# Kernel optimization log

Hardware: AMD Instinct MI355X
Metric: run time of the kernel (lower is better)

Reference implementation:

```python
import jax, jax.numpy as jnp
import numpy as np

N_NODES = 100000
N_EDGES = 1600000
D = 128
D_FF = 2 * D
BN_EPS = 1e-5


def setup_inputs() -> dict:
    key = jax.random.key(0)
    ks = jax.random.split(key, 16)
    s = lambda k, shp, fan: jax.random.normal(k, shp, jnp.float32) / np.float32(np.sqrt(fan))
    return {
        "x": jax.random.normal(ks[0], (N_NODES, D), jnp.float32),
        "edge_attr": jax.random.normal(ks[1], (N_EDGES, D), jnp.float32),
        "w1g": s(ks[2], (D, D), D),
        "b1g": jnp.zeros((D,), jnp.float32),
        "w2g": s(ks[3], (D, D), D),
        "b2g": jnp.zeros((D,), jnp.float32),
        "bn1_g": jax.random.uniform(ks[4], (D,), jnp.float32, 0.5, 1.5),
        "bn1_b": 0.1 * jax.random.normal(ks[5], (D,), jnp.float32),
        "ff_w1": s(ks[6], (D, D_FF), D),
        "ff_b1": jnp.zeros((D_FF,), jnp.float32),
        "ff_w2": s(ks[7], (D_FF, D), D_FF),
        "ff_b2": jnp.zeros((D,), jnp.float32),
        "bn2_g": jax.random.uniform(ks[8], (D,), jnp.float32, 0.5, 1.5),
        "bn2_b": 0.1 * jax.random.normal(ks[9], (D,), jnp.float32),
        "edge_index": jax.random.randint(ks[10], (2, N_EDGES), 0, N_NODES, jnp.int64 if jax.config.jax_enable_x64 else jnp.int32),
    }


def _batchnorm(h, gamma, beta):
    # training-mode BatchNorm1d: per-batch (node-axis) stats, biased variance
    mean = h.mean(axis=0)
    var = ((h - mean) ** 2).mean(axis=0)
    return gamma * (h - mean) * jax.lax.rsqrt(var + BN_EPS) + beta


def reference(x, edge_attr, w1g, b1g, w2g, b2g, bn1_g, bn1_b,
              ff_w1, ff_b1, ff_w2, ff_b2, bn2_g, bn2_b, edge_index):
    src, dst = edge_index[0], edge_index[1]
    # GINEConv message: relu(x_j + e_ij), scatter-sum into target nodes
    msg = jax.nn.relu(x[src] + edge_attr)                      # [E, D]
    agg = jax.ops.segment_sum(msg, dst, num_segments=N_NODES)  # [N, D]
    h = x + agg                                                # (1+eps)*x with eps=0
    # gin_nn: Linear -> ReLU -> Linear
    h = jax.nn.relu(h @ w1g + b1g) @ w2g + b2g
    h = jax.nn.relu(h)                                         # post-conv relu; dropout=identity (eval)
    h = x + h                                                  # residual
    h = _batchnorm(h, bn1_g, bn1_b)                            # norm1_local
    ff = jax.nn.relu(h @ ff_w1 + ff_b1) @ ff_w2 + ff_b2        # FFN block (dropouts identity)
    h = h + ff
    h = _batchnorm(h, bn2_g, bn2_b)                            # norm2
    return h
```

## Files before the change

kernel.cpp:

```cpp
#include <hip/hip_runtime.h>
#include <hip/hip_bf16.h>

#define NN 100000
#define NE 1600000
#define DD 128
#define DFF 256
#define BN_EPS 1e-5f
#define NND ((size_t)NN * DD)
#define NB_SCAN 391
#define NTILE 6250

typedef __attribute__((ext_vector_type(8))) short short8;
typedef __attribute__((ext_vector_type(4))) float f32x4;
typedef __attribute__((ext_vector_type(4))) unsigned short us4;

static __device__ __forceinline__ unsigned short f2bf(float f) {
  union { float f; unsigned u; } v; v.f = f;
  unsigned r = v.u + 0x7fffu + ((v.u >> 16) & 1u);
  return (unsigned short)(r >> 16);
}
static __device__ __forceinline__ float bf2f(unsigned short h) {
  union { unsigned u; float f; } v; v.u = ((unsigned)h) << 16;
  return v.f;
}

__global__ __launch_bounds__(256) void k_prep_misc(const float* __restrict__ x,
    unsigned short* __restrict__ xbf,
    const float* __restrict__ w1g, const float* __restrict__ w2g,
    const float* __restrict__ ffw1, const float* __restrict__ ffw2,
    unsigned short* __restrict__ w1t, unsigned short* __restrict__ w2t,
    unsigned short* __restrict__ fw1t, unsigned short* __restrict__ fw2t) {
  int b = blockIdx.x;
  if (b < 6250) {
    size_t base = ((size_t)b * 256u + threadIdx.x) * 8;
    const f32x4* xp = reinterpret_cast<const f32x4*>(x + base);
    f32x4 a0 = xp[0], a1 = xp[1];
    short8 o;
#pragma unroll
    for (int j = 0; j < 4; ++j) o[j] = (short)f2bf(a0[j]);
#pragma unroll
    for (int j = 0; j < 4; ++j) o[4 + j] = (short)f2bf(a1[j]);
    *reinterpret_cast<short8*>(xbf + base) = o;
  } else {
    int i = (b - 6250) * 256 + threadIdx.x;
    if (i < 16384) { int c = i & 127, k = i >> 7; w1t[c * 128 + k] = f2bf(w1g[k * 128 + c]); }
    else if (i < 32768) { i -= 16384; int c = i & 127, k = i >> 7; w2t[c * 128 + k] = f2bf(w2g[k * 128 + c]); }
    else if (i < 65536) { i -= 32768; int c = i & 255, k = i >> 8; fw1t[c * 128 + k] = f2bf(ffw1[k * 256 + c]); }
    else if (i < 98304) { i -= 65536; int c = i & 127, k = i >> 7; fw2t[c * 256 + k] = f2bf(ffw2[k * 128 + c]); }
  }
}

__global__ __launch_bounds__(256) void k_hist(const int* __restrict__ ei,
                                              int* __restrict__ cnt) {
  int e = blockIdx.x * 256 + threadIdx.x;
  if (e >= NE) return;
  atomicAdd(&cnt[ei[NE + e]], 1);
}

__global__ __launch_bounds__(256) void k_scan1(const int* __restrict__ cnt,
                                               int* __restrict__ bsum) {
  __shared__ int sh[256];
  int n = blockIdx.x * 256 + threadIdx.x;
  sh[threadIdx.x] = (n < NN) ? cnt[n] : 0;
  __syncthreads();
  for (int off = 128; off > 0; off >>= 1) {
    if (threadIdx.x < off) sh[threadIdx.x] += sh[threadIdx.x + off];
    __syncthreads();
  }
  if (threadIdx.x == 0) bsum[blockIdx.x] = sh[0];
}

__global__ __launch_bounds__(512) void k_scan2(const int* __restrict__ bsum,
                                               int* __restrict__ bpre,
                                               int* __restrict__ rs) {
  __shared__ int sh[512];
  int t = threadIdx.x;
  int v = (t < NB_SCAN) ? bsum[t] : 0;
  sh[t] = v;
  __syncthreads();
  for (int off = 1; off < 512; off <<= 1) {
    int u = (t >= off) ? sh[t - off] : 0;
    __syncthreads();
    sh[t] += u;
    __syncthreads();
  }
  if (t < NB_SCAN) bpre[t] = sh[t] - v;
  if (t == NB_SCAN - 1) rs[NN] = sh[t];
}

__global__ __launch_bounds__(256) void k_scan3(int* __restrict__ rs,
                                               const int* __restrict__ bpre,
                                               int* __restrict__ cursor) {
  __shared__ int sh[256];
  int n = blockIdx.x * 256 + threadIdx.x;
  int t = threadIdx.x;
  int v = (n < NN) ? rs[n] : 0;
  sh[t] = v;
  __syncthreads();
  for (int off = 1; off < 256; off <<= 1) {
    int u = (t >= off) ? sh[t - off] : 0;
    __syncthreads();
    sh[t] += u;
    __syncthreads();
  }
  if (n < NN) {
    int ex = bpre[blockIdx.x] + sh[t] - v;
    rs[n] = ex;
    cursor[n] = ex;
  }
}

__global__ __launch_bounds__(256) void k_scatter(const int* __restrict__ ei,
                                                 int* __restrict__ cursor,
                                                 int2* __restrict__ el2) {
  int e = blockIdx.x * 256 + threadIdx.x;
  if (e >= NE) return;
  int s = ei[e], d = ei[NE + e];
  int p = atomicAdd(&cursor[d], 1);
  el2[p] = make_int2(e, s);
}

__global__ __launch_bounds__(256) void k_gather(const float* __restrict__ x,
    const unsigned short* __restrict__ xbf, const float* __restrict__ ea,
    const int* __restrict__ rs, const int2* __restrict__ el2,
    unsigned short* __restrict__ h0) {
  int n = blockIdx.x * 8 + (threadIdx.x >> 5);
  int q = threadIdx.x & 31;
  int beg = rs[n], end = rs[n + 1];
  f32x4 acc = (f32x4){0.f, 0.f, 0.f, 0.f};
  int2 A = make_int2(0, 0), B = A;
  if (beg < end) A = el2[beg];
  if (beg + 1 < end) B = el2[beg + 1];
  int i = beg;
  for (; i + 2 <= end; i += 2) {
    f32x4 evA = *(reinterpret_cast<const f32x4*>(ea + (size_t)A.x * DD) + q);
    us4  xvA = *reinterpret_cast<const us4*>(xbf + (size_t)A.y * DD + q * 4);
    f32x4 evB = *(reinterpret_cast<const f32x4*>(ea + (size_t)B.x * DD) + q);
    us4  xvB = *reinterpret_cast<const us4*>(xbf + (size_t)B.y * DD + q * 4);
    int2 C = A, Dn = B;
    if (i + 2 < end) C = el2[i + 2];
    if (i + 3 < end) Dn = el2[i + 3];
#pragma unroll
    for (int c = 0; c < 4; ++c) {
      float mA = bf2f((unsigned short)xvA[c]) + evA[c];
      acc[c] += (mA > 0.f) ? mA : 0.f;
      float mB = bf2f((unsigned short)xvB[c]) + evB[c];
      acc[c] += (mB > 0.f) ? mB : 0.f;
    }
    A = C; B = Dn;
  }
  if (i < end) {
    f32x4 evA = *(reinterpret_cast<const f32x4*>(ea + (size_t)A.x * DD) + q);
    us4  xvA = *reinterpret_cast<const us4*>(xbf + (size_t)A.y * DD + q * 4);
#pragma unroll
    for (int c = 0; c < 4; ++c) {
      float mA = bf2f((unsigned short)xvA[c]) + evA[c];
      acc[c] += (mA > 0.f) ? mA : 0.f;
    }
  }
  f32x4 xn = *(reinterpret_cast<const f32x4*>(x + (size_t)n * DD) + q);
  union { unsigned short us[4]; unsigned long long u; } pk;
#pragma unroll
  for (int c = 0; c < 4; ++c) pk.us[c] = f2bf(xn[c] + acc[c]);
  *reinterpret_cast<unsigned long long*>(h0 + (size_t)n * DD + q * 4) = pk.u;
}

__global__ __launch_bounds__(256) void k_gemm1(const unsigned short* __restrict__ A,
    const unsigned short* __restrict__ WT, const float* __restrict__ bias,
    unsigned short* __restrict__ O) {
  int lane = threadIdx.x & 63, w = threadIdx.x >> 6;
  int tile = blockIdx.x * 4 + w;
  if (tile >= NTILE) return;
  int l15 = lane & 15, g = lane >> 4;
  int row0 = tile * 16;
  f32x4 acc[8];
#pragma unroll
  for (int ct = 0; ct < 8; ++ct) {
    float b = bias[ct * 16 + l15];
    acc[ct] = (f32x4){b, b, b, b};
  }
  short8 a[4];
#pragma unroll
  for (int kt = 0; kt < 4; ++kt)
    a[kt] = *reinterpret_cast<const short8*>(A + (size_t)(row0 + l15) * DD + kt * 32 + g * 8);
#pragma unroll
  for (int kt = 0; kt < 4; ++kt) {
    int k0 = kt * 32 + g * 8;
#pragma unroll
    for (int ct = 0; ct < 8; ++ct) {
      int c = ct * 16 + l15;
      short8 b = *reinterpret_cast<const short8*>(WT + (size_t)c * DD + k0);
      acc[ct] = __builtin_amdgcn_mfma_f32_16x16x32_bf16(a[kt], b, acc[ct], 0, 0, 0);
    }
  }
#pragma unroll
  for (int ct = 0; ct < 8; ++ct) {
    int c = ct * 16 + l15;
#pragma unroll
    for (int r = 0; r < 4; ++r) {
      int row = row0 + g * 4 + r;
      float v = acc[ct][r];
      v = v > 0.f ? v : 0.f;
      O[(size_t)row * DD + c] = f2bf(v);
    }
  }
}

__global__ __launch_bounds__(256) void k_gemm2(const unsigned short* __restrict__ A,
    const unsigned short* __restrict__ WT, const float* __restrict__ bias,
    const float* __restrict__ x, float* __restrict__ O, float* __restrict__ stats) {
  __shared__ float lds_s[128], lds_q[128];
  if (threadIdx.x < 128) { lds_s[threadIdx.x] = 0.f; lds_q[threadIdx.x] = 0.f; }
  __syncthreads();
  int lane = threadIdx.x & 63, w = threadIdx.x >> 6;
  int tile = blockIdx.x * 4 + w;
  int l15 = lane & 15, g = lane >> 4;
  if (tile < NTILE) {
    int row0 = tile * 16;
    f32x4 acc[8];
#pragma unroll
    for (int ct = 0; ct < 8; ++ct) {
      float b = bias[ct * 16 + l15];
      acc[ct] = (f32x4){b, b, b, b};
    }
    short8 a[4];
#pragma unroll
    for (int kt = 0; kt < 4; ++kt)
      a[kt] = *reinterpret_cast<const short8*>(A + (size_t)(row0 + l15) * DD + kt * 32 + g * 8);
#pragma unroll
    for (int kt = 0; kt < 4; ++kt) {
      int k0 = kt * 32 + g * 8;
#pragma unroll
      for (int ct = 0; ct < 8; ++ct) {
        int c = ct * 16 + l15;
        short8 b = *reinterpret_cast<const short8*>(WT + (size_t)c * DD + k0);
        acc[ct] = __builtin_amdgcn_mfma_f32_16x16x32_bf16(a[kt], b, acc[ct], 0, 0, 0);
      }
    }
#pragma unroll
    for (int ct = 0; ct < 8; ++ct) {
      int c = ct * 16 + l15;
      float s = 0.f, q = 0.f;
#pragma unroll
      for (int r = 0; r < 4; ++r) {
        int row = row0 + g * 4 + r;
        float v = acc[ct][r];
        v = v > 0.f ? v : 0.f;
        v += x[(size_t)row * DD + c];
        O[(size_t)row * DD + c] = v;
        s += v; q += v * v;
      }
      s += __shfl_xor(s, 16); s += __shfl_xor(s, 32);
      q += __shfl_xor(q, 16); q += __shfl_xor(q, 32);
      if (g == 0) { atomicAdd(&lds_s[c], s); atomicAdd(&lds_q[c], q); }
    }
  }
  __syncthreads();
  if (threadIdx.x < 128) {
    atomicAdd(&stats[threadIdx.x], lds_s[threadIdx.x]);
    atomicAdd(&stats[128 + threadIdx.x], lds_q[threadIdx.x]);
  }
}

__global__ void k_bnfin(const float* __restrict__ st, const float* __restrict__ gm,
                        const float* __restrict__ bt, float* __restrict__ par) {
  int c = threadIdx.x;
  float mean = st[c] * (1.f / NN);
  float var = st[128 + c] * (1.f / NN) - mean * mean;
  float sc = gm[c] * rsqrtf(var + BN_EPS);
  par[c] = sc;
  par[128 + c] = bt[c] - mean * sc;
}

__global__ __launch_bounds__(256) void k_gemm3(const float* __restrict__ H,
    const float* __restrict__ par, const unsigned short* __restrict__ WT,
    const float* __restrict__ bias, unsigned short* __restrict__ O) {
  int lane = threadIdx.x & 63, w = threadIdx.x >> 6;
  int colhalf = w & 1;
  int tile = blockIdx.x * 2 + (w >> 1);
  if (tile >= NTILE) return;
  int l15 = lane & 15, g = lane >> 4;
  int row0 = tile * 16;
  f32x4 acc[8];
#pragma unroll
  for (int ct = 0; ct < 8; ++ct) {
    float b = bias[colhalf * 128 + ct * 16 + l15];
    acc[ct] = (f32x4){b, b, b, b};
  }
  const float* arow = H + (size_t)(row0 + l15) * DD;
  short8 a[4];
#pragma unroll
  for (int kt = 0; kt < 4; ++kt) {
    int k0 = kt * 32 + g * 8;
    f32x4 u0 = *reinterpret_cast<const f32x4*>(arow + k0);
    f32x4 u1 = *reinterpret_cast<const f32x4*>(arow + k0 + 4);
    f32x4 sc0 = *reinterpret_cast<const f32x4*>(par + k0);
    f32x4 sc1 = *reinterpret_cast<const f32x4*>(par + k0 + 4);
    f32x4 sh0 = *reinterpret_cast<const f32x4*>(par + 128 + k0);
    f32x4 sh1 = *reinterpret_cast<const f32x4*>(par + 128 + k0 + 4);
    short8 af;
#pragma unroll
    for (int j = 0; j < 4; ++j) af[j] = (short)f2bf(sc0[j] * u0[j] + sh0[j]);
#pragma unroll
    for (int j = 0; j < 4; ++j) af[4 + j] = (short)f2bf(sc1[j] * u1[j] + sh1[j]);
    a[kt] = af;
  }
#pragma unroll
  for (int kt = 0; kt < 4; ++kt) {
    int k0 = kt * 32 + g * 8;
#pragma unroll
    for (int ct = 0; ct < 8; ++ct) {
      int c = colhalf * 128 + ct * 16 + l15;
      short8 b = *reinterpret_cast<const short8*>(WT + (size_t)c * DD + k0);
      acc[ct] = __builtin_amdgcn_mfma_f32_16x16x32_bf16(a[kt], b, acc[ct], 0, 0, 0);
    }
  }
#pragma unroll
  for (int ct = 0; ct < 8; ++ct) {
    int c = colhalf * 128 + ct * 16 + l15;
#pragma unroll
    for (int r = 0; r < 4; ++r) {
      int row = row0 + g * 4 + r;
      float v = acc[ct][r];
      v = v > 0.f ? v : 0.f;
      O[(size_t)row * DFF + c] = f2bf(v);
    }
  }
}

__global__ __launch_bounds__(256) void k_gemm4(const unsigned short* __restrict__ A,
    const unsigned short* __restrict__ WT, const float* __restrict__ bias,
    const float* __restrict__ par, float* __restrict__ O, float* __restrict__ stats) {
  __shared__ float lds_s[128], lds_q[128];
  if (threadIdx.x < 128) { lds_s[threadIdx.x] = 0.f; lds_q[threadIdx.x] = 0.f; }
  __syncthreads();
  int lane = threadIdx.x & 63, w = threadIdx.x >> 6;
  int tile = blockIdx.x * 4 + w;
  int l15 = lane & 15, g = lane >> 4;
  if (tile < NTILE) {
    int row0 = tile * 16;
    f32x4 acc[8];
#pragma unroll
    for (int ct = 0; ct < 8; ++ct) {
      float b = bias[ct * 16 + l15];
      acc[ct] = (f32x4){b, b, b, b};
    }
    short8 a[8];
#pragma unroll
    for (int kt = 0; kt < 8; ++kt)
      a[kt] = *reinterpret_cast<const short8*>(A + (size_t)(row0 + l15) * DFF + kt * 32 + g * 8);
#pragma unroll 2
    for (int kt = 0; kt < 8; ++kt) {
      int k0 = kt * 32 + g * 8;
#pragma unroll
      for (int ct = 0; ct < 8; ++ct) {
        int c = ct * 16 + l15;
        short8 b = *reinterpret_cast<const short8*>(WT + (size_t)c * DFF + k0);
        acc[ct] = __builtin_amdgcn_mfma_f32_16x16x32_bf16(a[kt], b, acc[ct], 0, 0, 0);
      }
    }
#pragma unroll
    for (int ct = 0; ct < 8; ++ct) {
      int c = ct * 16 + l15;
      float sc = par[c], sh = par[128 + c];
      float s = 0.f, q = 0.f;
#pragma unroll
      for (int r = 0; r < 4; ++r) {
        int row = row0 + g * 4 + r;
        float h1v = sc * O[(size_t)row * DD + c] + sh;
        float v = acc[ct][r] + h1v;
        O[(size_t)row * DD + c] = v;
        s += v; q += v * v;
      }
      s += __shfl_xor(s, 16); s += __shfl_xor(s, 32);
      q += __shfl_xor(q, 16); q += __shfl_xor(q, 32);
      if (g == 0) { atomicAdd(&lds_s[c], s); atomicAdd(&lds_q[c], q); }
    }
  }
  __syncthreads();
  if (threadIdx.x < 128) {
    atomicAdd(&stats[threadIdx.x], lds_s[threadIdx.x]);
    atomicAdd(&stats[128 + threadIdx.x], lds_q[threadIdx.x]);
  }
}

__global__ __launch_bounds__(256) void k_bnfinal(float* __restrict__ h,
    const float* __restrict__ st, const float* __restrict__ gm,
    const float* __restrict__ bt) {
  size_t base = ((size_t)blockIdx.x * 256u + threadIdx.x) * 4;
  int c0 = (int)(base & 127);
  f32x4 v = *reinterpret_cast<f32x4*>(h + base);
#pragma unroll
  for (int j = 0; j < 4; ++j) {
    int c = c0 + j;
    float mean = st[c] * (1.f / NN);
    float var = st[128 + c] * (1.f / NN) - mean * mean;
    float sc = gm[c] * rsqrtf(var + BN_EPS);
    float sh = bt[c] - mean * sc;
    v[j] = sc * v[j] + sh;
  }
  *reinterpret_cast<f32x4*>(h + base) = v;
}

extern "C" void kernel_launch(void* const* d_in, const int* in_sizes, int n_in,
                              void* d_out, int out_size, void* d_ws, size_t ws_size,
                              hipStream_t stream) {
  const float* x    = (const float*)d_in[0];
  const float* ea   = (const float*)d_in[1];
  const float* w1g  = (const float*)d_in[2];
  const float* b1g  = (const float*)d_in[3];
  const float* w2g  = (const float*)d_in[4];
  const float* b2g  = (const float*)d_in[5];
  const float* bn1g = (const float*)d_in[6];
  const float* bn1b = (const float*)d_in[7];
  const float* ffw1 = (const float*)d_in[8];
  const float* ffb1 = (const float*)d_in[9];
  const float* ffw2 = (const float*)d_in[10];
  const float* ffb2 = (const float*)d_in[11];
  const float* bn2g = (const float*)d_in[12];
  const float* bn2b = (const float*)d_in[13];
  const int*   eidx = (const int*)d_in[14];
  float* out = (float*)d_out;

  char* ws = (char*)d_ws;
  int2* el2    = (int2*)(ws);
  int*  rs     = (int*)(ws + 12800000);
  int*  cursor = (int*)(ws + 13200128);
  int*  bsum   = (int*)(ws + 13600128);
  int*  bpre   = (int*)(ws + 13601728);
  float* stats = (float*)(ws + 13603328);
  float* par   = (float*)(ws + 13605376);
  unsigned short* w1t  = (unsigned short*)(ws + 13607424);
  unsigned short* w2t  = w1t + 16384;
  unsigned short* fw1t = w2t + 16384;
  unsigned short* fw2t = fw1t + 32768;
  unsigned short* xbf  = (unsigned short*)(ws + 13804032);
  unsigned short* hbf  = (unsigned short*)(ws + 39404032);
  unsigned short* r1bf = (unsigned short*)(ws + 65004032);
  unsigned short* f1bf = (unsigned short*)(ws + 90604032);

  hipMemsetAsync(rs, 0, (NN + 1) * 4, stream);
  hipMemsetAsync(stats, 0, 512 * 4, stream);

  k_prep_misc<<<6634, 256, 0, stream>>>(x, xbf, w1g, w2g, ffw1, ffw2,
                                        w1t, w2t, fw1t, fw2t);

  k_hist<<<6250, 256, 0, stream>>>(eidx, rs);
  k_scan1<<<NB_SCAN, 256, 0, stream>>>(rs, bsum);
  k_scan2<<<1, 512, 0, stream>>>(bsum, bpre, rs);
  k_scan3<<<NB_SCAN, 256, 0, stream>>>(rs, bpre, cursor);
  k_scatter<<<6250, 256, 0, stream>>>(eidx, cursor, el2);

  k_gather<<<12500, 256, 0, stream>>>(x, xbf, ea, rs, el2, hbf);

  k_gemm1<<<1563, 256, 0, stream>>>(hbf, w1t, b1g, r1bf);
  k_gemm2<<<1563, 256, 0, stream>>>(r1bf, w2t, b2g, x, out, stats);
  k_bnfin<<<1, 128, 0, stream>>>(stats, bn1g, bn1b, par);
  k_gemm3<<<3125, 256, 0, stream>>>(out, par, fw1t, ffb1, f1bf);
  k_gemm4<<<1563, 256, 0, stream>>>(f1bf, fw2t, ffb2, par, out, stats + 256);
  k_bnfinal<<<12500, 256, 0, stream>>>(out, stats + 256, bn2g, bn2b);
}
```

Baseline: 755.3 us.

## Fuse GEMM pairs via LDS and unroll edge gather to four edges

The two GIN MLP GEMMs and the two FFN GEMMs are each merged into a single kernel. The ReLU'd bf16 intermediate stays in a padded per-wave LDS tile instead of going through global memory, which removes the r1bf/f1bf round trips and two launches. The gather loop now keeps four edges in flight instead of two to raise memory-level parallelism. The self term now reads x in bf16 rather than fp32, which cuts bytes but adds rounding error. The fused FFN kernel holds 16 accumulators and uses more LDS, which may lower occupancy.

```diff
diff --git a/kernel.cpp b/kernel.cpp
--- a/kernel.cpp
+++ b/kernel.cpp
@@ -120,7 +120,7 @@
   el2[p] = make_int2(e, s);
 }
 
-__global__ __launch_bounds__(256) void k_gather(const float* __restrict__ x,
+__global__ __launch_bounds__(256) void k_gather(
     const unsigned short* __restrict__ xbf, const float* __restrict__ ea,
     const int* __restrict__ rs, const int2* __restrict__ el2,
     unsigned short* __restrict__ h0) {
@@ -128,99 +128,91 @@
   int q = threadIdx.x & 31;
   int beg = rs[n], end = rs[n + 1];
   f32x4 acc = (f32x4){0.f, 0.f, 0.f, 0.f};
-  int2 A = make_int2(0, 0), B = A;
-  if (beg < end) A = el2[beg];
-  if (beg + 1 < end) B = el2[beg + 1];
+  int2 E0 = make_int2(0, 0), E1 = E0, E2 = E0, E3 = E0;
   int i = beg;
-  for (; i + 2 <= end; i += 2) {
-    f32x4 evA = *(reinterpret_cast<const f32x4*>(ea + (size_t)A.x * DD) + q);
-    us4  xvA = *reinterpret_cast<const us4*>(xbf + (size_t)A.y * DD + q * 4);
-    f32x4 evB = *(reinterpret_cast<const f32x4*>(ea + (size_t)B.x * DD) + q);
-    us4  xvB = *reinterpret_cast<const us4*>(xbf + (size_t)B.y * DD + q * 4);
-    int2 C = A, Dn = B;
-    if (i + 2 < end) C = el2[i + 2];
-    if (i + 3 < end) Dn = el2[i + 3];
+  if (i     < end) E0 = el2[i];
+  if (i + 1 < end) E1 = el2[i + 1];
+  if (i + 2 < end) E2 = el2[i + 2];
+  if (i + 3 < end) E3 = el2[i + 3];
+  for (; i + 4 <= end; i += 4) {
+    f32x4 ev0 = *(reinterpret_cast<const f32x4*>(ea + (size_t)E0.x * DD) + q);
+    us4  xv0 = *reinterpret_cast<const us4*>(xbf + (size_t)E0.y * DD + q * 4);
+    f32x4 ev1 = *(reinterpret_cast<const f32x4*>(ea + (size_t)E1.x * DD) + q);
+    us4  xv1 = *reinterpret_cast<const us4*>(xbf + (size_t)E1.y * DD + q * 4);
+    f32x4 ev2 = *(reinterpret_cast<const f32x4*>(ea + (size_t)E2.x * DD) + q);
+    us4  xv2 = *reinterpret_cast<const us4*>(xbf + (size_t)E2.y * DD + q * 4);
+    f32x4 ev3 = *(reinterpret_cast<const f32x4*>(ea + (size_t)E3.x * DD) + q);
+    us4  xv3 = *reinterpret_cast<const us4*>(xbf + (size_t)E3.y * DD + q * 4);
+    int2 N0 = E0, N1 = E1, N2 = E2, N3 = E3;
+    if (i + 4 < end) N0 = el2[i + 4];
+    if (i + 5 < end) N1 = el2[i + 5];
+    if (i + 6 < end) N2 = el2[i + 6];
+    if (i + 7 < end) N3 = el2[i + 7];
 #pragma unroll
     for (int c = 0; c < 4; ++c) {
-      float mA = bf2f((unsigned short)xvA[c]) + evA[c];
-      acc[c] += (mA > 0.f) ? mA : 0.f;
-      float mB = bf2f((unsigned short)xvB[c]) + evB[c];
-      acc[c] += (mB > 0.f) ? mB : 0.f;
-    }
-    A = C; B = Dn;
+      float m0 = bf2f((unsigned short)xv0[c]) + ev0[c];
+      acc[c] += (m0 > 0.f) ? m0 : 0.f;
+      float m1 = bf2f((unsigned short)xv1[c]) + ev1[c];
+      acc[c] += (m1 > 0.f) ? m1 : 0.f;
+      float m2 = bf2f((unsigned short)xv2[c]) + ev2[c];
+      acc[c] += (m2 > 0.f) ? m2 : 0.f;
+      float m3 = bf2f((unsigned short)xv3[c]) + ev3[c];
+      acc[c] += (m3 > 0.f) ? m3 : 0.f;
+    }
+    E0 = N0; E1 = N1; E2 = N2; E3 = N3;
   }
   if (i < end) {
-    f32x4 evA = *(reinterpret_cast<const f32x4*>(ea + (size_t)A.x * DD) + q);
-    us4  xvA = *reinterpret_cast<const us4*>(xbf + (size_t)A.y * DD + q * 4);
+    f32x4 ev = *(reinterpret_cast<const f32x4*>(ea + (size_t)E0.x * DD) + q);
+    us4  xv = *reinterpret_cast<const us4*>(xbf + (size_t)E0.y * DD + q * 4);
 #pragma unroll
     for (int c = 0; c < 4; ++c) {
-      float mA = bf2f((unsigned short)xvA[c]) + evA[c];
-      acc[c] += (mA > 0.f) ? mA : 0.f;
-    }
-  }
-  f32x4 xn = *(reinterpret_cast<const f32x4*>(x + (size_t)n * DD) + q);
+      float m = bf2f((unsigned short)xv[c]) + ev[c];
+      acc[c] += (m > 0.f) ? m : 0.f;
+    }
+  }
+  if (i + 1 < end) {
+    f32x4 ev = *(reinterpret_cast<const f32x4*>(ea + (size_t)E1.x * DD) + q);
+    us4  xv = *reinterpret_cast<const us4*>(xbf + (size_t)E1.y * DD + q * 4);
+#pragma unroll
+    for (int c = 0; c < 4; ++c) {
+      float m = bf2f((unsigned short)xv[c]) + ev[c];
+      acc[c] += (m > 0.f) ? m : 0.f;
+    }
+  }
+  if (i + 2 < end) {
+    f32x4 ev = *(reinterpret_cast<const f32x4*>(ea + (size_t)E2.x * DD) + q);
+    us4  xv = *reinterpret_cast<const us4*>(xbf + (size_t)E2.y * DD + q * 4);
+#pragma unroll
+    for (int c = 0; c < 4; ++c) {
+      float m = bf2f((unsigned short)xv[c]) + ev[c];
+      acc[c] += (m > 0.f) ? m : 0.f;
+    }
+  }
+  us4 xs = *reinterpret_cast<const us4*>(xbf + (size_t)n * DD + q * 4);
   union { unsigned short us[4]; unsigned long long u; } pk;
 #pragma unroll
-  for (int c = 0; c < 4; ++c) pk.us[c] = f2bf(xn[c] + acc[c]);
+  for (int c = 0; c < 4; ++c) pk.us[c] = f2bf(bf2f((unsigned short)xs[c]) + acc[c]);
   *reinterpret_cast<unsigned long long*>(h0 + (size_t)n * DD + q * 4) = pk.u;
 }
 
-__global__ __launch_bounds__(256) void k_gemm1(const unsigned short* __restrict__ A,
-    const unsigned short* __restrict__ WT, const float* __restrict__ bias,
-    unsigned short* __restrict__ O) {
-  int lane = threadIdx.x & 63, w = threadIdx.x >> 6;
-  int tile = blockIdx.x * 4 + w;
-  if (tile >= NTILE) return;
-  int l15 = lane & 15, g = lane >> 4;
-  int row0 = tile * 16;
-  f32x4 acc[8];
-#pragma unroll
-  for (int ct = 0; ct < 8; ++ct) {
-    float b = bias[ct * 16 + l15];
-    acc[ct] = (f32x4){b, b, b, b};
-  }
-  short8 a[4];
-#pragma unroll
-  for (int kt = 0; kt < 4; ++kt)
-    a[kt] = *reinterpret_cast<const short8*>(A + (size_t)(row0 + l15) * DD + kt * 32 + g * 8);
-#pragma unroll
-  for (int kt = 0; kt < 4; ++kt) {
-    int k0 = kt * 32 + g * 8;
-#pragma unroll
-    for (int ct = 0; ct < 8; ++ct) {
-      int c = ct * 16 + l15;
-      short8 b = *reinterpret_cast<const short8*>(WT + (size_t)c * DD + k0);
-      acc[ct] = __builtin_amdgcn_mfma_f32_16x16x32_bf16(a[kt], b, acc[ct], 0, 0, 0);
-    }
-  }
-#pragma unroll
-  for (int ct = 0; ct < 8; ++ct) {
-    int c = ct * 16 + l15;
-#pragma unroll
-    for (int r = 0; r < 4; ++r) {
-      int row = row0 + g * 4 + r;
-      float v = acc[ct][r];
-      v = v > 0.f ? v : 0.f;
-      O[(size_t)row * DD + c] = f2bf(v);
-    }
-  }
-}
-
-__global__ __launch_bounds__(256) void k_gemm2(const unsigned short* __restrict__ A,
-    const unsigned short* __restrict__ WT, const float* __restrict__ bias,
+#define TR1 136
+__global__ __launch_bounds__(256) void k_mlp1(const unsigned short* __restrict__ A,
+    const unsigned short* __restrict__ W1T, const float* __restrict__ b1,
+    const unsigned short* __restrict__ W2T, const float* __restrict__ b2,
     const float* __restrict__ x, float* __restrict__ O, float* __restrict__ stats) {
+  __shared__ unsigned short tr[4][16 * TR1];
   __shared__ float lds_s[128], lds_q[128];
   if (threadIdx.x < 128) { lds_s[threadIdx.x] = 0.f; lds_q[threadIdx.x] = 0.f; }
-  __syncthreads();
   int lane = threadIdx.x & 63, w = threadIdx.x >> 6;
   int tile = blockIdx.x * 4 + w;
   int l15 = lane & 15, g = lane >> 4;
+  int row0 = tile * 16;
+  __syncthreads();
   if (tile < NTILE) {
-    int row0 = tile * 16;
     f32x4 acc[8];
 #pragma unroll
     for (int ct = 0; ct < 8; ++ct) {
-      float b = bias[ct * 16 + l15];
+      float b = b1[ct * 16 + l15];
       acc[ct] = (f32x4){b, b, b, b};
     }
     short8 a[4];
@@ -233,8 +225,40 @@
 #pragma unroll
       for (int ct = 0; ct < 8; ++ct) {
         int c = ct * 16 + l15;
-        short8 b = *reinterpret_cast<const short8*>(WT + (size_t)c * DD + k0);
+        short8 b = *reinterpret_cast<const short8*>(W1T + (size_t)c * DD + k0);
         acc[ct] = __builtin_amdgcn_mfma_f32_16x16x32_bf16(a[kt], b, acc[ct], 0, 0, 0);
+      }
+    }
+#pragma unroll
+    for (int ct = 0; ct < 8; ++ct) {
+#pragma unroll
+      for (int r = 0; r < 4; ++r) {
+        float v = acc[ct][r];
+        v = v > 0.f ? v : 0.f;
+        tr[w][(g * 4 + r) * TR1 + ct * 16 + l15] = f2bf(v);
+      }
+    }
+  }
+  __syncthreads();
+  if (tile < NTILE) {
+    short8 a2[4];
+#pragma unroll
+    for (int kt = 0; kt < 4; ++kt)
+      a2[kt] = *reinterpret_cast<const short8*>(&tr[w][l15 * TR1 + kt * 32 + g * 8]);
+    f32x4 acc2[8];
+#pragma unroll
+    for (int ct = 0; ct < 8; ++ct) {
+      float b = b2[ct * 16 + l15];
+      acc2[ct] = (f32x4){b, b, b, b};
+    }
+#pragma unroll
+    for (int kt = 0; kt < 4; ++kt) {
+      int k0 = kt * 32 + g * 8;
+#pragma unroll
+      for (int ct = 0; ct < 8; ++ct) {
+        int c = ct * 16 + l15;
+        short8 b = *reinterpret_cast<const short8*>(W2T + (size_t)c * DD + k0);
+        acc2[ct] = __builtin_amdgcn_mfma_f32_16x16x32_bf16(a2[kt], b, acc2[ct], 0, 0, 0);
       }
     }
 #pragma unroll
@@ -244,7 +268,7 @@
 #pragma unroll
       for (int r = 0; r < 4; ++r) {
         int row = row0 + g * 4 + r;
-        float v = acc[ct][r];
+        float v = acc2[ct][r];
         v = v > 0.f ? v : 0.f;
         v += x[(size_t)row * DD + c];
         O[(size_t)row * DD + c] = v;
@@ -272,91 +296,84 @@
   par[128 + c] = bt[c] - mean * sc;
 }
 
-__global__ __launch_bounds__(256) void k_gemm3(const float* __restrict__ H,
-    const float* __restrict__ par, const unsigned short* __restrict__ WT,
-    const float* __restrict__ bias, unsigned short* __restrict__ O) {
-  int lane = threadIdx.x & 63, w = threadIdx.x >> 6;
-  int colhalf = w & 1;
-  int tile = blockIdx.x * 2 + (w >> 1);
-  if (tile >= NTILE) return;
-  int l15 = lane & 15, g = lane >> 4;
-  int row0 = tile * 16;
-  f32x4 acc[8];
-#pragma unroll
-  for (int ct = 0; ct < 8; ++ct) {
-    float b = bias[colhalf * 128 + ct * 16 + l15];
-    acc[ct] = (f32x4){b, b, b, b};
-  }
-  const float* arow = H + (size_t)(row0 + l15) * DD;
-  short8 a[4];
-#pragma unroll
-  for (int kt = 0; kt < 4; ++kt) {
-    int k0 = kt * 32 + g * 8;
-    f32x4 u0 = *reinterpret_cast<const f32x4*>(arow + k0);
-    f32x4 u1 = *reinterpret_cast<const f32x4*>(arow + k0 + 4);
-    f32x4 sc0 = *reinterpret_cast<const f32x4*>(par + k0);
-    f32x4 sc1 = *reinterpret_cast<const f32x4*>(par + k0 + 4);
-    f32x4 sh0 = *reinterpret_cast<const f32x4*>(par + 128 + k0);
-    f32x4 sh1 = *reinterpret_cast<const f32x4*>(par + 128 + k0 + 4);
-    short8 af;
-#pragma unroll
-    for (int j = 0; j < 4; ++j) af[j] = (short)f2bf(sc0[j] * u0[j] + sh0[j]);
-#pragma unroll
-    for (int j = 0; j < 4; ++j) af[4 + j] = (short)f2bf(sc1[j] * u1[j] + sh1[j]);
-    a[kt] = af;
-  }
-#pragma unroll
-  for (int kt = 0; kt < 4; ++kt) {
-    int k0 = kt * 32 + g * 8;
-#pragma unroll
-    for (int ct = 0; ct < 8; ++ct) {
-      int c = colhalf * 128 + ct * 16 + l15;
-      short8 b = *reinterpret_cast<const short8*>(WT + (size_t)c * DD + k0);
-      acc[ct] = __builtin_amdgcn_mfma_f32_16x16x32_bf16(a[kt], b, acc[ct], 0, 0, 0);
-    }
-  }
-#pragma unroll
-  for (int ct = 0; ct < 8; ++ct) {
-    int c = colhalf * 128 + ct * 16 + l15;
-#pragma unroll
-    for (int r = 0; r < 4; ++r) {
-      int row = row0 + g * 4 + r;
-      float v = acc[ct][r];
-      v = v > 0.f ? v : 0.f;
-      O[(size_t)row * DFF + c] = f2bf(v);
-    }
-  }
-}
-
-__global__ __launch_bounds__(256) void k_gemm4(const unsigned short* __restrict__ A,
-    const unsigned short* __restrict__ WT, const float* __restrict__ bias,
-    const float* __restrict__ par, float* __restrict__ O, float* __restrict__ stats) {
+#define TR2 264
+__global__ __launch_bounds__(256) void k_mlp2(const float* __restrict__ H,
+    const float* __restrict__ par, const unsigned short* __restrict__ FW1T,
+    const float* __restrict__ fb1, const unsigned short* __restrict__ FW2T,
+    const float* __restrict__ fb2, float* __restrict__ O, float* __restrict__ stats) {
+  __shared__ unsigned short tr[4][16 * TR2];
   __shared__ float lds_s[128], lds_q[128];
   if (threadIdx.x < 128) { lds_s[threadIdx.x] = 0.f; lds_q[threadIdx.x] = 0.f; }
-  __syncthreads();
   int lane = threadIdx.x & 63, w = threadIdx.x >> 6;
   int tile = blockIdx.x * 4 + w;
   int l15 = lane & 15, g = lane >> 4;
+  int row0 = tile * 16;
+  __syncthreads();
   if (tile < NTILE) {
-    int row0 = tile * 16;
-    f32x4 acc[8];
-#pragma unroll
-    for (int ct = 0; ct < 8; ++ct) {
-      float b = bias[ct * 16 + l15];
-      acc[ct] = (f32x4){b, b, b, b};
-    }
-    short8 a[8];
+    const float* arow = H + (size_t)(row0 + l15) * DD;
+    short8 a1[4];
+#pragma unroll
+    for (int kt = 0; kt < 4; ++kt) {
+      int k0 = kt * 32 + g * 8;
+      f32x4 u0 = *reinterpret_cast<const f32x4*>(arow + k0);
+      f32x4 u1 = *reinterpret_cast<const f32x4*>(arow + k0 + 4);
+      f32x4 sc0 = *reinterpret_cast<const f32x4*>(par + k0);
+      f32x4 sc1 = *reinterpret_cast<const f32x4*>(par + k0 + 4);
+      f32x4 sh0 = *reinterpret_cast<const f32x4*>(par + 128 + k0);
+      f32x4 sh1 = *reinterpret_cast<const f32x4*>(par + 128 + k0 + 4);
+      short8 af;
+#pragma unroll
+      for (int j = 0; j < 4; ++j) af[j] = (short)f2bf(sc0[j] * u0[j] + sh0[j]);
+#pragma unroll
+      for (int j = 0; j < 4; ++j) af[4 + j] = (short)f2bf(sc1[j] * u1[j] + sh1[j]);
+      a1[kt] = af;
+    }
+    f32x4 acc1[16];
+#pragma unroll
+    for (int ct = 0; ct < 16; ++ct) {
+      float b = fb1[ct * 16 + l15];
+      acc1[ct] = (f32x4){b, b, b, b};
+    }
+#pragma unroll
+    for (int kt = 0; kt < 4; ++kt) {
+      int k0 = kt * 32 + g * 8;
+#pragma unroll
+      for (int ct = 0; ct < 16; ++ct) {
+        int c = ct * 16 + l15;
+        short8 b = *reinterpret_cast<const short8*>(FW1T + (size_t)c * DD + k0);
+        acc1[ct] = __builtin_amdgcn_mfma_f32_16x16x32_bf16(a1[kt], b, acc1[ct], 0, 0, 0);
+      }
+    }
+#pragma unroll
+    for (int ct = 0; ct < 16; ++ct) {
+#pragma unroll
+      for (int r = 0; r < 4; ++r) {
+        float v = acc1[ct][r];
+        v = v > 0.f ? v : 0.f;
+        tr[w][(g * 4 + r) * TR2 + ct * 16 + l15] = f2bf(v);
+      }
+    }
+  }
+  __syncthreads();
+  if (tile < NTILE) {
+    short8 a2[8];
 #pragma unroll
     for (int kt = 0; kt < 8; ++kt)
-      a[kt] = *reinterpret_cast<const short8*>(A + (size_t)(row0 + l15) * DFF + kt * 32 + g * 8);
+      a2[kt] = *reinterpret_cast<const short8*>(&tr[w][l15 * TR2 + kt * 32 + g * 8]);
+    f32x4 acc2[8];
+#pragma unroll
+    for (int ct = 0; ct < 8; ++ct) {
+      float b = fb2[ct * 16 + l15];
+      acc2[ct] = (f32x4){b, b, b, b};
+    }
 #pragma unroll 2
     for (int kt = 0; kt < 8; ++kt) {
       int k0 = kt * 32 + g * 8;
 #pragma unroll
       for (int ct = 0; ct < 8; ++ct) {
         int c = ct * 16 + l15;
-        short8 b = *reinterpret_cast<const short8*>(WT + (size_t)c * DFF + k0);
-        acc[ct] = __builtin_amdgcn_mfma_f32_16x16x32_bf16(a[kt], b, acc[ct], 0, 0, 0);
+        short8 b = *reinterpret_cast<const short8*>(FW2T + (size_t)c * DFF + k0);
+        acc2[ct] = __builtin_amdgcn_mfma_f32_16x16x32_bf16(a2[kt], b, acc2[ct], 0, 0, 0);
       }
     }
 #pragma unroll
@@ -368,7 +385,7 @@
       for (int r = 0; r < 4; ++r) {
         int row = row0 + g * 4 + r;
         float h1v = sc * O[(size_t)row * DD + c] + sh;
-        float v = acc[ct][r] + h1v;
+        float v = acc2[ct][r] + h1v;
         O[(size_t)row * DD + c] = v;
         s += v; q += v * v;
       }
@@ -436,8 +453,6 @@
   unsigned short* fw2t = fw1t + 32768;
   unsigned short* xbf  = (unsigned short*)(ws + 13804032);
   unsigned short* hbf  = (unsigned short*)(ws + 39404032);
-  unsigned short* r1bf = (unsigned short*)(ws + 65004032);
-  unsigned short* f1bf = (unsigned short*)(ws + 90604032);
 
   hipMemsetAsync(rs, 0, (NN + 1) * 4, stream);
   hipMemsetAsync(stats, 0, 512 * 4, stream);
@@ -451,12 +466,10 @@
   k_scan3<<<NB_SCAN, 256, 0, stream>>>(rs, bpre, cursor);
   k_scatter<<<6250, 256, 0, stream>>>(eidx, cursor, el2);
 
-  k_gather<<<12500, 256, 0, stream>>>(x, xbf, ea, rs, el2, hbf);
-
-  k_gemm1<<<1563, 256, 0, stream>>>(hbf, w1t, b1g, r1bf);
-  k_gemm2<<<1563, 256, 0, stream>>>(r1bf, w2t, b2g, x, out, stats);
+  k_gather<<<12500, 256, 0, stream>>>(xbf, ea, rs, el2, hbf);
+
+  k_mlp1<<<1563, 256, 0, stream>>>(hbf, w1t, b1g, w2t, b2g, x, out, stats);
   k_bnfin<<<1, 128, 0, stream>>>(stats, bn1g, bn1b, par);
-  k_gemm3<<<3125, 256, 0, stream>>>(out, par, fw1t, ffb1, f1bf);
-  k_gemm4<<<1563, 256, 0, stream>>>(f1bf, fw2t, ffb2, par, out, stats + 256);
+  k_mlp2<<<1563, 256, 0, stream>>>(out, par, fw1t, ffb1, fw2t, ffb2, out, stats + 256);
   k_bnfinal<<<12500, 256, 0, stream>>>(out, stats + 256, bn2g, bn2b);
 }
```

Result: faster. 722.0 us (-4.4%).
